# Kernel optimization log

Hardware: AMD Instinct MI355X
Metric: run time of the kernel (lower is better)

The kernel has to match this reference:

```python
import jax, jax.numpy as jnp
import numpy as np

NUM_LAYERS = 4  # -> 9 blocks: 4 encoder + bottleneck + 4 decoder
EPS = 1e-6
SQRT2 = float(np.sqrt(2.0))
INV_SQRT3 = float(1.0 / np.sqrt(3.0))


def _block(s, v, W0, W1, Wa, Wb):
    """_SelfInteractionUNet with full_square=False, irreps = Mx0e + Mx1o.

    tensor_square of per-channel (0e+1o):
      0e: s*s ; 0e: |v|^2/sqrt(3) ; 1o: sqrt(2)*s*v ; (2e is produced by e3nn
      but irreps_out has no 2e so the Linear discards it -> omitted here).
    """
    M = s.shape[-1]
    ts0a = s * s                                    # [N, M] 0e
    ts0b = jnp.sum(v * v, axis=-1) * INV_SQRT3      # [N, M] 0e
    ts1 = SQRT2 * s[..., None] * v                  # [N, M, 3] 1o
    s_in = jnp.concatenate([s, ts0a, ts0b], axis=-1)   # [N, 3M]
    v_in = jnp.concatenate([v, ts1], axis=1)           # [N, 2M, 3]
    # irreps-segmented Linear with path (fan-in) normalization
    s2 = (s_in @ W0) * (1.0 / np.sqrt(s_in.shape[-1]))               # [N, Mo]
    v2 = jnp.einsum('ncd,co->nod', v_in, W1) * (1.0 / np.sqrt(v_in.shape[1]))  # [N, Mo, 3]
    Mo = W0.shape[-1]
    # gated MLP on invariants (0e part), silu after each layer
    h = jax.nn.silu((s2 @ Wa) * (1.0 / np.sqrt(Mo)))                 # [N, Mo]
    g = jax.nn.silu((h @ Wb) * (1.0 / np.sqrt(Mo)))                  # [N, 2Mo]
    s2 = s2 * g[:, :Mo]
    v2 = v2 * g[:, Mo:, None]
    return s2, v2


def _eq_layernorm(s, v):
    # scalars: center + RMS normalize; vectors: norm-RMS normalize (equivariant)
    s = s - jnp.mean(s, axis=-1, keepdims=True)
    s = s * jax.lax.rsqrt(jnp.mean(s * s, axis=-1, keepdims=True) + EPS)
    v = v * jax.lax.rsqrt(jnp.mean(v * v, axis=(1, 2), keepdims=True) + EPS)
    return s, v


def _unet(scalars, vectors, W0, W1, Wa, Wb):
    s, v = scalars, vectors
    skips = []
    for i in range(NUM_LAYERS):
        s, v = _block(s, v, W0[i], W1[i], Wa[i], Wb[i])
        s, v = _eq_layernorm(s, v)
        skips.append((s, v))
    s, v = _block(s, v, W0[NUM_LAYERS], W1[NUM_LAYERS], Wa[NUM_LAYERS], Wb[NUM_LAYERS])
    for j in range(NUM_LAYERS):
        ss, vs = skips[NUM_LAYERS - 1 - j]
        s, v = s + ss, v + vs
        k = NUM_LAYERS + 1 + j
        s, v = _block(s, v, W0[k], W1[k], Wa[k], Wb[k])
        if j < NUM_LAYERS - 1:  # no norm on last decoder layer (norm_last=False)
            s, v = _eq_layernorm(s, v)
    N = s.shape[0]
    return jnp.concatenate([s, v.reshape(N, -1)], axis=-1)  # [N, 4M] irreps_array layout


def setup_inputs() -> dict:
    key = jax.random.key(0)
    ks = jax.random.split(key, 6)
    N, M = 16384, 256
    return {
        'scalars': jax.random.normal(ks[0], (N, M), jnp.float32),
        'vectors': jax.random.normal(ks[1], (N, M, 3), jnp.float32),
        'W0': jax.random.normal(ks[2], (9, 3 * M, M), jnp.float32),
        'W1': jax.random.normal(ks[3], (9, 2 * M, M), jnp.float32),
        'Wa': jax.random.normal(ks[4], (9, M, M), jnp.float32),
        'Wb': jax.random.normal(ks[5], (9, M, 2 * M), jnp.float32),
    }


def reference(scalars, vectors, W0, W1, Wa, Wb):
    return _unet(scalars, vectors, W0, W1, Wa, Wb)
```

## Files before the change

kernel.cpp:

```cpp
#include <hip/hip_runtime.h>
#include <hip/hip_bf16.h>
#include <math.h>


typedef __attribute__((ext_vector_type(8))) short bf16x8;
typedef __attribute__((ext_vector_type(4))) short bf16x4;
typedef __attribute__((ext_vector_type(4))) float f32x4;
typedef __attribute__((ext_vector_type(4))) _Float16 f16x4;

__device__ __forceinline__ unsigned asu(float f){ union{float f;unsigned u;}x; x.f=f; return x.u; }
__device__ __forceinline__ float asf(unsigned u){ union{unsigned u;float f;}x; x.u=u; return x.f; }

__device__ __forceinline__ unsigned short f2bf_r(float f){
  unsigned i = asu(f);
  return (unsigned short)((i + 0x7fffu + ((i >> 16) & 1u)) >> 16);
}
__device__ __forceinline__ float bf2f(unsigned short u){ return asf(((unsigned)u) << 16); }

__device__ __forceinline__ void split_t(float f, short& hi, short& lo){
  unsigned u = asu(f);
  hi = (short)(u >> 16);
  float lof = f - asf(u & 0xffff0000u);
  lo = (short)(asu(lof) >> 16);
}
__device__ __forceinline__ float rec(short h, short l){
  return asf(((unsigned)(unsigned short)h) << 16) + asf(((unsigned)(unsigned short)l) << 16);
}
__device__ __forceinline__ f32x4 rec4(const unsigned short* H, const unsigned short* L, size_t o){
  bf16x4 hv = *(const bf16x4*)(H + o);
  bf16x4 lv = *(const bf16x4*)(L + o);
  f32x4 f;
  #pragma unroll
  for (int j = 0; j < 4; ++j) f[j] = rec(hv[j], lv[j]);
  return f;
}

__device__ __forceinline__ int LO(int r, int kc){
  return r * 32 + ((((kc >> 3) ^ (r & 3)) << 3) | (kc & 7));
}

__global__ __launch_bounds__(256)
void transpose_w(const float* __restrict__ W, unsigned short* __restrict__ Wh,
                 unsigned short* __restrict__ Wl, int K, int Mo){
  __shared__ float tile[32][33];
  const int bi = blockIdx.z;
  const float* Wb = W + (size_t)bi * K * Mo;
  const size_t wo = (size_t)bi * K * Mo;
  const int k0 = blockIdx.x * 32, o0 = blockIdx.y * 32;
  const int tx = threadIdx.x & 31, ty = threadIdx.x >> 5;
  #pragma unroll
  for (int i = 0; i < 4; ++i){
    int k = ty + i * 8;
    tile[k][tx] = Wb[(size_t)(k0 + k) * Mo + o0 + tx];
  }
  __syncthreads();
  #pragma unroll
  for (int i = 0; i < 4; ++i){
    int o = ty + i * 8;
    float f = tile[tx][o];
    unsigned short h = f2bf_r(f);
    unsigned short l = f2bf_r(f - bf2f(h));
    Wh[wo + (size_t)(o0 + o) * K + k0 + tx] = h;
    Wl[wo + (size_t)(o0 + o) * K + k0 + tx] = l;
  }
}

__global__ __launch_bounds__(256)
void convert_inputs(const float* __restrict__ s, const float* __restrict__ v,
                    unsigned short* __restrict__ stH, unsigned short* __restrict__ stL,
                    int NM){
  int i = blockIdx.x * 256 + threadIdx.x;
  if (i >= NM) return;
  short h, l;
  split_t(s[i], h, l); stH[i] = h; stL[i] = l;
  const float* vp = v + (size_t)i * 3;
  #pragma unroll
  for (int d = 0; d < 3; ++d){
    split_t(vp[d], h, l);
    stH[(size_t)(1 + d) * NM + i] = h;
    stL[(size_t)(1 + d) * NM + i] = l;
  }
}

__global__ __launch_bounds__(512, 8)
void gemm_sv(const unsigned short* __restrict__ StH, const unsigned short* __restrict__ StL,
             const _Float16* __restrict__ skip,
             const unsigned short* __restrict__ W0h, const unsigned short* __restrict__ W0l,
             const unsigned short* __restrict__ W1h, const unsigned short* __restrict__ W1l,
             unsigned short* __restrict__ s2H, unsigned short* __restrict__ s2L,
             unsigned short* __restrict__ v2H, unsigned short* __restrict__ v2L,
             int NM, float cs, float cv)
{
  __shared__ unsigned short Ash[64*32], Asl[64*32], Bsh[256*32], Bsl[256*32];
  const int tid = threadIdx.x;
  const int lane = tid & 63, wave = tid >> 6;
  const int wm = (wave >> 2) * 32, wn = (wave & 3) * 64;
  const int row0 = blockIdx.x * 64;
  const int z = blockIdx.y;
  const bool isS = (z == 0);
  const int dv = z - 1;
  const int K = isS ? 768 : 512;
  const float scale = isS ? cs : cv;
  const unsigned short* Bhg = isS ? W0h : W1h;
  const unsigned short* Blg = isS ? W0l : W1l;
  unsigned short* outH = isS ? s2H : v2H + (size_t)dv * NM;
  unsigned short* outL = isS ? s2L : v2L + (size_t)dv * NM;
  const bool sk = (skip != nullptr);

  f32x4 acc[2][4];
  #pragma unroll
  for (int m = 0; m < 2; ++m){
    #pragma unroll
    for (int n = 0; n < 4; ++n) acc[m][n] = (f32x4){0.f,0.f,0.f,0.f};
  }

  const int bc = tid >> 1, bk = (tid & 1) * 16;
  const int ar = tid >> 3, ac = (tid & 7) * 4;

  for (int k0 = 0; k0 < K; k0 += 32){
    {
      const size_t o = (size_t)bc * K + k0 + bk;
      bf16x8 x0 = *(const bf16x8*)(Bhg + o);
      bf16x8 x1 = *(const bf16x8*)(Bhg + o + 8);
      bf16x8 y0 = *(const bf16x8*)(Blg + o);
      bf16x8 y1 = *(const bf16x8*)(Blg + o + 8);
      *(bf16x8*)(&Bsh[LO(bc, bk)])     = x0;
      *(bf16x8*)(&Bsh[LO(bc, bk + 8)]) = x1;
      *(bf16x8*)(&Bsl[LO(bc, bk)])     = y0;
      *(bf16x8*)(&Bsl[LO(bc, bk + 8)]) = y1;
    }
    {
      const int gr = row0 + ar;
      const int c  = (k0 + ac) & 255;
      const size_t o = (size_t)gr * 256 + c;
      const int seg = k0 >> 8;
      if (!sk && seg == 0){
        const int p = isS ? 0 : 1 + dv;
        *(bf16x4*)(&Ash[LO(ar, ac)]) = *(const bf16x4*)(StH + (size_t)p * NM + o);
        *(bf16x4*)(&Asl[LO(ar, ac)]) = *(const bf16x4*)(StL + (size_t)p * NM + o);
      } else {
        f32x4 f;
        if (isS){
          if (seg <= 1){
            f32x4 x = rec4(StH, StL, o);
            if (sk){
              f16x4 y = *(const f16x4*)(skip + o);
              #pragma unroll
              for (int j = 0; j < 4; ++j) x[j] += (float)y[j];
            }
            if (seg == 0){
              f = x;
            } else {
              #pragma unroll
              for (int j = 0; j < 4; ++j) f[j] = x[j] * x[j];
            }
          } else {
            f32x4 a0 = rec4(StH, StL, (size_t)NM + o);
            f32x4 a1 = rec4(StH, StL, (size_t)2*NM + o);
            f32x4 a2 = rec4(StH, StL, (size_t)3*NM + o);
            if (sk){
              f16x4 b0 = *(const f16x4*)(skip + (size_t)NM + o);
              f16x4 b1 = *(const f16x4*)(skip + (size_t)2*NM + o);
              f16x4 b2 = *(const f16x4*)(skip + (size_t)3*NM + o);
              #pragma unroll
              for (int j = 0; j < 4; ++j){
                a0[j] += (float)b0[j]; a1[j] += (float)b1[j]; a2[j] += (float)b2[j];
              }
            }
            #pragma unroll
            for (int j = 0; j < 4; ++j)
              f[j] = (a0[j]*a0[j] + a1[j]*a1[j] + a2[j]*a2[j]) * 0.57735026918962576f;
          }
        } else {
          f32x4 x = rec4(StH, StL, (size_t)(1 + dv)*NM + o);
          if (sk){
            f16x4 y = *(const f16x4*)(skip + (size_t)(1 + dv)*NM + o);
            #pragma unroll
            for (int j = 0; j < 4; ++j) x[j] += (float)y[j];
          }
          if (seg == 0){
            f = x;
          } else {
            f32x4 s = rec4(StH, StL, o);
            if (sk){
              f16x4 y = *(const f16x4*)(skip + o);
              #pragma unroll
              for (int j = 0; j < 4; ++j) s[j] += (float)y[j];
            }
            #pragma unroll
            for (int j = 0; j < 4; ++j) f[j] = 1.41421356237309505f * s[j] * x[j];
          }
        }
        bf16x4 hi, lo;
        #pragma unroll
        for (int j = 0; j < 4; ++j){ short h, l; split_t(f[j], h, l); hi[j]=h; lo[j]=l; }
        *(bf16x4*)(&Ash[LO(ar, ac)]) = hi;
        *(bf16x4*)(&Asl[LO(ar, ac)]) = lo;
      }
    }
    __syncthreads();

    const int arow = lane & 15;
    const int kq   = (lane >> 4) * 8;
    bf16x8 ah[2], al[2], bh[4], bl[4];
    #pragma unroll
    for (int m = 0; m < 2; ++m){
      const int r = wm + m*16 + arow;
      ah[m] = *(const bf16x8*)(&Ash[LO(r, kq)]);
      al[m] = *(const bf16x8*)(&Asl[LO(r, kq)]);
    }
    #pragma unroll
    for (int n = 0; n < 4; ++n){
      const int r = wn + n*16 + arow;
      bh[n] = *(const bf16x8*)(&Bsh[LO(r, kq)]);
      bl[n] = *(const bf16x8*)(&Bsl[LO(r, kq)]);
    }
    #pragma unroll
    for (int m = 0; m < 2; ++m){
      #pragma unroll
      for (int n = 0; n < 4; ++n){
        acc[m][n] = __builtin_amdgcn_mfma_f32_16x16x32_bf16(ah[m], bh[n], acc[m][n], 0, 0, 0);
        acc[m][n] = __builtin_amdgcn_mfma_f32_16x16x32_bf16(al[m], bh[n], acc[m][n], 0, 0, 0);
        acc[m][n] = __builtin_amdgcn_mfma_f32_16x16x32_bf16(ah[m], bl[n], acc[m][n], 0, 0, 0);
      }
    }
    __syncthreads();
  }

  #pragma unroll
  for (int m = 0; m < 2; ++m){
    #pragma unroll
    for (int n = 0; n < 4; ++n){
      const int cg = wn + n*16 + (lane & 15);
      #pragma unroll
      for (int j = 0; j < 4; ++j){
        const int rg = row0 + wm + m*16 + ((lane >> 4) * 4) + j;
        short h, l; split_t(acc[m][n][j] * scale, h, l);
        outH[(size_t)rg * 256 + cg] = (unsigned short)h;
        outL[(size_t)rg * 256 + cg] = (unsigned short)l;
      }
    }
  }
}

template<int EPI>
__global__ __launch_bounds__(512, 8)
void gemm_hg(const unsigned short* __restrict__ AhG, const unsigned short* __restrict__ AlG,
             const unsigned short* __restrict__ Bh, const unsigned short* __restrict__ Bl,
             int NM, float scale,
             unsigned short* __restrict__ outH, unsigned short* __restrict__ outL,
             const unsigned short* __restrict__ s2H, const unsigned short* __restrict__ s2L,
             const unsigned short* __restrict__ v2H, const unsigned short* __restrict__ v2L,
             unsigned short* __restrict__ stH, unsigned short* __restrict__ stL,
             float* __restrict__ fout)
{
  __shared__ unsigned short Ash[32*32], Asl[32*32], Bsh[256*32], Bsl[256*32];
  const int tid = threadIdx.x;
  const int lane = tid & 63, wave = tid >> 6;
  const int wm = (wave >> 2) * 16, wn = (wave & 3) * 64;
  const int row0 = blockIdx.x * 32;
  const int col0 = blockIdx.y * 256;
  const int K = 256;

  f32x4 acc[2][4];
  #pragma unroll
  for (int m = 0; m < 2; ++m){
    #pragma unroll
    for (int n = 0; n < 4; ++n) acc[m][n] = (f32x4){0.f,0.f,0.f,0.f};
  }

  const int bc = tid >> 1, bk = (tid & 1) * 16;

  for (int k0 = 0; k0 < K; k0 += 32){
    {
      const size_t o = (size_t)(col0 + bc) * K + k0 + bk;
      bf16x8 x0 = *(const bf16x8*)(Bh + o);
      bf16x8 x1 = *(const bf16x8*)(Bh + o + 8);
      bf16x8 y0 = *(const bf16x8*)(Bl + o);
      bf16x8 y1 = *(const bf16x8*)(Bl + o + 8);
      *(bf16x8*)(&Bsh[LO(bc, bk)])     = x0;
      *(bf16x8*)(&Bsh[LO(bc, bk + 8)]) = x1;
      *(bf16x8*)(&Bsl[LO(bc, bk)])     = y0;
      *(bf16x8*)(&Bsl[LO(bc, bk + 8)]) = y1;
    }
    if (tid < 256){
      const int ar = tid >> 3, ac = (tid & 7) * 4;
      const size_t o = (size_t)(row0 + ar) * 256 + k0 + ac;
      *(bf16x4*)(&Ash[LO(ar, ac)]) = *(const bf16x4*)(AhG + o);
      *(bf16x4*)(&Asl[LO(ar, ac)]) = *(const bf16x4*)(AlG + o);
    }
    __syncthreads();

    const int arow = lane & 15;
    const int kq   = (lane >> 4) * 8;
    bf16x8 ah, al, bh[4], bl[4];
    {
      const int r = wm + arow;
      ah = *(const bf16x8*)(&Ash[LO(r, kq)]);
      al = *(const bf16x8*)(&Asl[LO(r, kq)]);
    }
    #pragma unroll
    for (int n = 0; n < 4; ++n){
      const int r = wn + n*16 + arow;
      bh[n] = *(const bf16x8*)(&Bsh[LO(r, kq)]);
      bl[n] = *(const bf16x8*)(&Bsl[LO(r, kq)]);
    }
    #pragma unroll
    for (int n = 0; n < 4; ++n){
      acc[0][n] = __builtin_amdgcn_mfma_f32_16x16x32_bf16(ah, bh[n], acc[0][n], 0, 0, 0);
      acc[0][n] = __builtin_amdgcn_mfma_f32_16x16x32_bf16(al, bh[n], acc[0][n], 0, 0, 0);
      acc[0][n] = __builtin_amdgcn_mfma_f32_16x16x32_bf16(ah, bl[n], acc[0][n], 0, 0, 0);
    }
    __syncthreads();
  }

  #pragma unroll
  for (int n = 0; n < 4; ++n){
    const int cg = col0 + wn + n*16 + (lane & 15);
    #pragma unroll
    for (int j = 0; j < 4; ++j){
      const int rg = row0 + wm + ((lane >> 4) * 4) + j;
      float val = acc[0][n][j] * scale;
      if (EPI == 1){
        float sl = val / (1.f + expf(-val));
        short h, l; split_t(sl, h, l);
        outH[(size_t)rg * 256 + cg] = (unsigned short)h;
        outL[(size_t)rg * 256 + cg] = (unsigned short)l;
      } else {
        float gv = val / (1.f + expf(-val));
        if (cg < 256){
          const size_t o = (size_t)rg * 256 + cg;
          float sval = rec(s2H[o], s2L[o]) * gv;
          if (EPI == 2){
            short h, l; split_t(sval, h, l);
            stH[o] = (unsigned short)h; stL[o] = (unsigned short)l;
          } else {
            fout[(size_t)rg * 1024 + cg] = sval;
          }
        } else {
          const int c = cg - 256;
          #pragma unroll
          for (int d = 0; d < 3; ++d){
            const size_t o = (size_t)d * NM + (size_t)rg * 256 + c;
            float vv = rec(v2H[o], v2L[o]) * gv;
            if (EPI == 2){
              short h, l; split_t(vv, h, l);
              stH[(size_t)(1+d) * NM + (size_t)rg * 256 + c] = (unsigned short)h;
              stL[(size_t)(1+d) * NM + (size_t)rg * 256 + c] = (unsigned short)l;
            } else {
              fout[(size_t)rg * 1024 + 256 + 3 * (size_t)c + d] = vv;
            }
          }
        }
      }
    }
  }
}

__global__ __launch_bounds__(256)
void ln_k(unsigned short* __restrict__ stH, unsigned short* __restrict__ stL,
          _Float16* __restrict__ snap, int NM){
  const int row  = blockIdx.x * 4 + (threadIdx.x >> 6);
  const int lane = threadIdx.x & 63;
  const size_t o = (size_t)row * 256 + lane * 4;
  f32x4 sv = rec4(stH, stL, o);
  f32x4 v0 = rec4(stH, stL, (size_t)NM + o);
  f32x4 v1 = rec4(stH, stL, (size_t)2*NM + o);
  f32x4 v2 = rec4(stH, stL, (size_t)3*NM + o);
  float r0 = 0.f, r1 = 0.f, r2 = 0.f;
  #pragma unroll
  for (int j = 0; j < 4; ++j){
    r0 += sv[j];
    r1 += sv[j] * sv[j];
    r2 += v0[j]*v0[j] + v1[j]*v1[j] + v2[j]*v2[j];
  }
  #pragma unroll
  for (int off = 1; off < 64; off <<= 1){
    r0 += __shfl_xor(r0, off, 64);
    r1 += __shfl_xor(r1, off, 64);
    r2 += __shfl_xor(r2, off, 64);
  }
  float mu  = r0 * (1.f / 256.f);
  float var = r1 * (1.f / 256.f) - mu * mu;
  float srs = rsqrtf(var + 1e-6f);
  float vrs = rsqrtf(r2 * (1.f / 768.f) + 1e-6f);
  f32x4 pl[4];
  #pragma unroll
  for (int j = 0; j < 4; ++j){
    pl[0][j] = (sv[j] - mu) * srs;
    pl[1][j] = v0[j] * vrs; pl[2][j] = v1[j] * vrs; pl[3][j] = v2[j] * vrs;
  }
  #pragma unroll
  for (int p = 0; p < 4; ++p){
    bf16x4 hv, lv; f16x4 hx;
    #pragma unroll
    for (int j = 0; j < 4; ++j){
      short h, l; split_t(pl[p][j], h, l);
      hv[j] = h; lv[j] = l; hx[j] = (_Float16)pl[p][j];
    }
    *(bf16x4*)(stH + (size_t)p*NM + o) = hv;
    *(bf16x4*)(stL + (size_t)p*NM + o) = lv;
    if (snap) *(f16x4*)(snap + (size_t)p*NM + o) = hx;
  }
}

extern "C" void kernel_launch(void* const* d_in, const int* in_sizes, int n_in,
                              void* d_out, int out_size, void* d_ws, size_t ws_size,
                              hipStream_t stream){
  const float* s_in = (const float*)d_in[0];
  const float* v_in = (const float*)d_in[1];
  const float* W0 = (const float*)d_in[2];
  const float* W1 = (const float*)d_in[3];
  const float* Wa = (const float*)d_in[4];
  const float* Wb = (const float*)d_in[5];
  const int Mdim = 256;
  const int N  = in_sizes[0] / Mdim;
  const int NM = N * Mdim;

  unsigned short* ws = (unsigned short*)d_ws;
  size_t off = 0;
  auto alloc = [&](size_t elems){ unsigned short* p = ws + off; off += elems; return p; };
  unsigned short* W0h = alloc((size_t)9 * 768 * 256);
  unsigned short* W0l = alloc((size_t)9 * 768 * 256);
  unsigned short* W1h = alloc((size_t)9 * 512 * 256);
  unsigned short* W1l = alloc((size_t)9 * 512 * 256);
  unsigned short* Wah = alloc((size_t)9 * 256 * 256);
  unsigned short* Wal = alloc((size_t)9 * 256 * 256);
  unsigned short* Wbh = alloc((size_t)9 * 256 * 512);
  unsigned short* Wbl = alloc((size_t)9 * 256 * 512);
  unsigned short* s2H = alloc(NM);
  unsigned short* s2L = alloc(NM);
  unsigned short* v2H = alloc((size_t)3 * NM);
  unsigned short* v2L = alloc((size_t)3 * NM);
  unsigned short* hH  = alloc(NM);
  unsigned short* hL  = alloc(NM);
  _Float16* skips = (_Float16*)(ws + off);
  (void)ws_size;

  unsigned short* stateH = (unsigned short*)d_out;
  unsigned short* stateL = stateH + (size_t)4 * NM;

  dim3 blk(256);
  dim3 blk5(512);
  transpose_w<<<dim3(768/32, 256/32, 9), blk, 0, stream>>>(W0, W0h, W0l, 768, 256);
  transpose_w<<<dim3(512/32, 256/32, 9), blk, 0, stream>>>(W1, W1h, W1l, 512, 256);
  transpose_w<<<dim3(256/32, 256/32, 9), blk, 0, stream>>>(Wa, Wah, Wal, 256, 256);
  transpose_w<<<dim3(256/32, 512/32, 9), blk, 0, stream>>>(Wb, Wbh, Wbl, 256, 512);
  convert_inputs<<<dim3(NM/256), blk, 0, stream>>>(s_in, v_in, stateH, stateL, NM);

  const float c_s2 = 1.f / sqrtf(768.f);
  const float c_v2 = 1.f / sqrtf(512.f);
  const float c_hg = 1.f / 16.f;

  auto run_block = [&](int i, const _Float16* skip, bool fin){
    const unsigned short* w0h = W0h + (size_t)i * 768 * 256;
    const unsigned short* w0l = W0l + (size_t)i * 768 * 256;
    const unsigned short* w1h = W1h + (size_t)i * 512 * 256;
    const unsigned short* w1l = W1l + (size_t)i * 512 * 256;
    const unsigned short* wah = Wah + (size_t)i * 256 * 256;
    const unsigned short* wal = Wal + (size_t)i * 256 * 256;
    const unsigned short* wbh = Wbh + (size_t)i * 256 * 512;
    const unsigned short* wbl = Wbl + (size_t)i * 256 * 512;
    gemm_sv<<<dim3(N/64, 4), blk5, 0, stream>>>(stateH, stateL, skip,
                                                w0h, w0l, w1h, w1l,
                                                s2H, s2L, v2H, v2L, NM, c_s2, c_v2);
    gemm_hg<1><<<dim3(N/32, 1), blk5, 0, stream>>>(s2H, s2L, wah, wal, NM, c_hg,
                                                   hH, hL, nullptr, nullptr, nullptr, nullptr,
                                                   nullptr, nullptr, nullptr);
    if (!fin)
      gemm_hg<2><<<dim3(N/32, 2), blk5, 0, stream>>>(hH, hL, wbh, wbl, NM, c_hg,
                                                     nullptr, nullptr, s2H, s2L, v2H, v2L,
                                                     stateH, stateL, nullptr);
    else
      gemm_hg<3><<<dim3(N/32, 2), blk5, 0, stream>>>(hH, hL, wbh, wbl, NM, c_hg,
                                                     nullptr, nullptr, s2H, s2L, v2H, v2L,
                                                     nullptr, nullptr, (float*)d_out);
  };

  for (int i = 0; i < 4; ++i){
    run_block(i, nullptr, false);
    ln_k<<<dim3(N/4), blk, 0, stream>>>(stateH, stateL, skips + (size_t)i * 4 * NM, NM);
  }
  run_block(4, nullptr, false);
  for (int j = 0; j < 4; ++j){
    run_block(5 + j, skips + (size_t)(3 - j) * 4 * NM, j == 3);
    if (j < 3) ln_k<<<dim3(N/4), blk, 0, stream>>>(stateH, stateL, nullptr, NM);
  }
}
```

Measured before the change: 2.413 ms.

## Double GEMM row tiles, pad LDS rows, and use nontemporal global accesses

Doubles the M tile of gemm_sv (64 to 128 rows) and gemm_hg (32 to 64 rows) so each B tile loaded into LDS is reused across more rows. This halves the grid and lowers launch-bound occupancy to 4. The XOR-swizzled LDS layout is replaced by rows padded to stride 40, and the MFMA loop now loads A fragments per m. Most global loads and stores of activations and state become nontemporal, to keep the streaming traffic out of cache. The cost is more registers for the accumulators, more LDS, and fewer resident waves.

After: 3.778 ms. 1.57x slower.

```diff
diff --git a/kernel.cpp b/kernel.cpp
--- a/kernel.cpp
+++ b/kernel.cpp
@@ -26,18 +26,26 @@
 __device__ __forceinline__ float rec(short h, short l){
   return asf(((unsigned)(unsigned short)h) << 16) + asf(((unsigned)(unsigned short)l) << 16);
 }
-__device__ __forceinline__ f32x4 rec4(const unsigned short* H, const unsigned short* L, size_t o){
-  bf16x4 hv = *(const bf16x4*)(H + o);
-  bf16x4 lv = *(const bf16x4*)(L + o);
+
+__device__ __forceinline__ bf16x8 ntl8(const unsigned short* p){
+  return __builtin_nontemporal_load((const bf16x8*)p);
+}
+__device__ __forceinline__ bf16x4 ntl4(const unsigned short* p){
+  return __builtin_nontemporal_load((const bf16x4*)p);
+}
+__device__ __forceinline__ f16x4 ntlh(const _Float16* p){
+  return __builtin_nontemporal_load((const f16x4*)p);
+}
+__device__ __forceinline__ f32x4 rec4nt(const unsigned short* H, const unsigned short* L, size_t o){
+  bf16x4 hv = ntl4(H + o);
+  bf16x4 lv = ntl4(L + o);
   f32x4 f;
   #pragma unroll
   for (int j = 0; j < 4; ++j) f[j] = rec(hv[j], lv[j]);
   return f;
 }
 
-__device__ __forceinline__ int LO(int r, int kc){
-  return r * 32 + ((((kc >> 3) ^ (r & 3)) << 3) | (kc & 7));
-}
+__device__ __forceinline__ int LO(int r, int kc){ return r * 40 + kc; }
 
 __global__ __launch_bounds__(256)
 void transpose_w(const float* __restrict__ W, unsigned short* __restrict__ Wh,
@@ -82,7 +90,7 @@
   }
 }
 
-__global__ __launch_bounds__(512, 8)
+__global__ __launch_bounds__(512, 4)
 void gemm_sv(const unsigned short* __restrict__ StH, const unsigned short* __restrict__ StL,
              const _Float16* __restrict__ skip,
              const unsigned short* __restrict__ W0h, const unsigned short* __restrict__ W0l,
@@ -91,11 +99,11 @@
              unsigned short* __restrict__ v2H, unsigned short* __restrict__ v2L,
              int NM, float cs, float cv)
 {
-  __shared__ unsigned short Ash[64*32], Asl[64*32], Bsh[256*32], Bsl[256*32];
+  __shared__ unsigned short Ash[128*40], Asl[128*40], Bsh[256*40], Bsl[256*40];
   const int tid = threadIdx.x;
   const int lane = tid & 63, wave = tid >> 6;
-  const int wm = (wave >> 2) * 32, wn = (wave & 3) * 64;
-  const int row0 = blockIdx.x * 64;
+  const int wm = (wave >> 2) * 64, wn = (wave & 3) * 64;
+  const int row0 = blockIdx.x * 128;
   const int z = blockIdx.y;
   const bool isS = (z == 0);
   const int dv = z - 1;
@@ -107,17 +115,18 @@
   unsigned short* outL = isS ? s2L : v2L + (size_t)dv * NM;
   const bool sk = (skip != nullptr);
 
-  f32x4 acc[2][4];
-  #pragma unroll
-  for (int m = 0; m < 2; ++m){
+  f32x4 acc[4][4];
+  #pragma unroll
+  for (int m = 0; m < 4; ++m){
     #pragma unroll
     for (int n = 0; n < 4; ++n) acc[m][n] = (f32x4){0.f,0.f,0.f,0.f};
   }
 
   const int bc = tid >> 1, bk = (tid & 1) * 16;
-  const int ar = tid >> 3, ac = (tid & 7) * 4;
+  const int ar = tid >> 2, ac = (tid & 3) * 8;
 
   for (int k0 = 0; k0 < K; k0 += 32){
+    const int seg = k0 >> 8;
     {
       const size_t o = (size_t)bc * K + k0 + bk;
       bf16x8 x0 = *(const bf16x8*)(Bhg + o);
@@ -133,82 +142,79 @@
       const int gr = row0 + ar;
       const int c  = (k0 + ac) & 255;
       const size_t o = (size_t)gr * 256 + c;
-      const int seg = k0 >> 8;
       if (!sk && seg == 0){
         const int p = isS ? 0 : 1 + dv;
-        *(bf16x4*)(&Ash[LO(ar, ac)]) = *(const bf16x4*)(StH + (size_t)p * NM + o);
-        *(bf16x4*)(&Asl[LO(ar, ac)]) = *(const bf16x4*)(StL + (size_t)p * NM + o);
+        *(bf16x8*)(&Ash[LO(ar, ac)]) = ntl8(StH + (size_t)p * NM + o);
+        *(bf16x8*)(&Asl[LO(ar, ac)]) = ntl8(StL + (size_t)p * NM + o);
       } else {
-        f32x4 f;
-        if (isS){
-          if (seg <= 1){
-            f32x4 x = rec4(StH, StL, o);
+        #pragma unroll
+        for (int q = 0; q < 2; ++q){
+          const size_t oq = o + 4 * q;
+          f32x4 f;
+          if (isS){
+            if (seg <= 1){
+              f32x4 x = rec4nt(StH, StL, oq);
+              if (sk){
+                f16x4 y = ntlh(skip + oq);
+                #pragma unroll
+                for (int j = 0; j < 4; ++j) x[j] += (float)y[j];
+              }
+              if (seg == 0){
+                f = x;
+              } else {
+                #pragma unroll
+                for (int j = 0; j < 4; ++j) f[j] = x[j] * x[j];
+              }
+            } else {
+              f32x4 a0 = rec4nt(StH, StL, (size_t)NM + oq);
+              f32x4 a1 = rec4nt(StH, StL, (size_t)2*NM + oq);
+              f32x4 a2 = rec4nt(StH, StL, (size_t)3*NM + oq);
+              if (sk){
+                f16x4 b0 = ntlh(skip + (size_t)NM + oq);
+                f16x4 b1 = ntlh(skip + (size_t)2*NM + oq);
+                f16x4 b2 = ntlh(skip + (size_t)3*NM + oq);
+                #pragma unroll
+                for (int j = 0; j < 4; ++j){
+                  a0[j] += (float)b0[j]; a1[j] += (float)b1[j]; a2[j] += (float)b2[j];
+                }
+              }
+              #pragma unroll
+              for (int j = 0; j < 4; ++j)
+                f[j] = (a0[j]*a0[j] + a1[j]*a1[j] + a2[j]*a2[j]) * 0.57735026918962576f;
+            }
+          } else {
+            f32x4 x = rec4nt(StH, StL, (size_t)(1 + dv)*NM + oq);
             if (sk){
-              f16x4 y = *(const f16x4*)(skip + o);
+              f16x4 y = ntlh(skip + (size_t)(1 + dv)*NM + oq);
               #pragma unroll
               for (int j = 0; j < 4; ++j) x[j] += (float)y[j];
             }
             if (seg == 0){
               f = x;
             } else {
+              f32x4 s = rec4nt(StH, StL, oq);
+              if (sk){
+                f16x4 y = ntlh(skip + oq);
+                #pragma unroll
+                for (int j = 0; j < 4; ++j) s[j] += (float)y[j];
+              }
               #pragma unroll
-              for (int j = 0; j < 4; ++j) f[j] = x[j] * x[j];
+              for (int j = 0; j < 4; ++j) f[j] = 1.41421356237309505f * s[j] * x[j];
             }
-          } else {
-            f32x4 a0 = rec4(StH, StL, (size_t)NM + o);
-            f32x4 a1 = rec4(StH, StL, (size_t)2*NM + o);
-            f32x4 a2 = rec4(StH, StL, (size_t)3*NM + o);
-            if (sk){
-              f16x4 b0 = *(const f16x4*)(skip + (size_t)NM + o);
-              f16x4 b1 = *(const f16x4*)(skip + (size_t)2*NM + o);
-              f16x4 b2 = *(const f16x4*)(skip + (size_t)3*NM + o);
-              #pragma unroll
-              for (int j = 0; j < 4; ++j){
-                a0[j] += (float)b0[j]; a1[j] += (float)b1[j]; a2[j] += (float)b2[j];
-              }
-            }
-            #pragma unroll
-            for (int j = 0; j < 4; ++j)
-              f[j] = (a0[j]*a0[j] + a1[j]*a1[j] + a2[j]*a2[j]) * 0.57735026918962576f;
           }
-        } else {
-          f32x4 x = rec4(StH, StL, (size_t)(1 + dv)*NM + o);
-          if (sk){
-            f16x4 y = *(const f16x4*)(skip + (size_t)(1 + dv)*NM + o);
-            #pragma unroll
-            for (int j = 0; j < 4; ++j) x[j] += (float)y[j];
-          }
-          if (seg == 0){
-            f = x;
-          } else {
-            f32x4 s = rec4(StH, StL, o);
-            if (sk){
-              f16x4 y = *(const f16x4*)(skip + o);
-              #pragma unroll
-              for (int j = 0; j < 4; ++j) s[j] += (float)y[j];
-            }
-            #pragma unroll
-            for (int j = 0; j < 4; ++j) f[j] = 1.41421356237309505f * s[j] * x[j];
-          }
+          bf16x4 hi, lo;
+          #pragma unroll
+          for (int j = 0; j < 4; ++j){ short h, l; split_t(f[j], h, l); hi[j]=h; lo[j]=l; }
+          *(bf16x4*)(&Ash[LO(ar, ac + 4*q)]) = hi;
+          *(bf16x4*)(&Asl[LO(ar, ac + 4*q)]) = lo;
         }
-        bf16x4 hi, lo;
-        #pragma unroll
-        for (int j = 0; j < 4; ++j){ short h, l; split_t(f[j], h, l); hi[j]=h; lo[j]=l; }
-        *(bf16x4*)(&Ash[LO(ar, ac)]) = hi;
-        *(bf16x4*)(&Asl[LO(ar, ac)]) = lo;
       }
     }
     __syncthreads();
 
     const int arow = lane & 15;
     const int kq   = (lane >> 4) * 8;
-    bf16x8 ah[2], al[2], bh[4], bl[4];
-    #pragma unroll
-    for (int m = 0; m < 2; ++m){
-      const int r = wm + m*16 + arow;
-      ah[m] = *(const bf16x8*)(&Ash[LO(r, kq)]);
-      al[m] = *(const bf16x8*)(&Asl[LO(r, kq)]);
-    }
+    bf16x8 bh[4], bl[4];
     #pragma unroll
     for (int n = 0; n < 4; ++n){
       const int r = wn + n*16 + arow;
@@ -216,19 +222,25 @@
       bl[n] = *(const bf16x8*)(&Bsl[LO(r, kq)]);
     }
     #pragma unroll
-    for (int m = 0; m < 2; ++m){
-      #pragma unroll
-      for (int n = 0; n < 4; ++n){
-        acc[m][n] = __builtin_amdgcn_mfma_f32_16x16x32_bf16(ah[m], bh[n], acc[m][n], 0, 0, 0);
-        acc[m][n] = __builtin_amdgcn_mfma_f32_16x16x32_bf16(al[m], bh[n], acc[m][n], 0, 0, 0);
-        acc[m][n] = __builtin_amdgcn_mfma_f32_16x16x32_bf16(ah[m], bl[n], acc[m][n], 0, 0, 0);
-      }
+    for (int m = 0; m < 4; ++m){
+      const int r = wm + m*16 + arow;
+      bf16x8 ah = *(const bf16x8*)(&Ash[LO(r, kq)]);
+      bf16x8 al = *(const bf16x8*)(&Asl[LO(r, kq)]);
+      #pragma unroll
+      for (int n = 0; n < 4; ++n)
+        acc[m][n] = __builtin_amdgcn_mfma_f32_16x16x32_bf16(ah, bh[n], acc[m][n], 0, 0, 0);
+      #pragma unroll
+      for (int n = 0; n < 4; ++n)
+        acc[m][n] = __builtin_amdgcn_mfma_f32_16x16x32_bf16(al, bh[n], acc[m][n], 0, 0, 0);
+      #pragma unroll
+      for (int n = 0; n < 4; ++n)
+        acc[m][n] = __builtin_amdgcn_mfma_f32_16x16x32_bf16(ah, bl[n], acc[m][n], 0, 0, 0);
     }
     __syncthreads();
   }
 
   #pragma unroll
-  for (int m = 0; m < 2; ++m){
+  for (int m = 0; m < 4; ++m){
     #pragma unroll
     for (int n = 0; n < 4; ++n){
       const int cg = wn + n*16 + (lane & 15);
@@ -236,15 +248,15 @@
       for (int j = 0; j < 4; ++j){
         const int rg = row0 + wm + m*16 + ((lane >> 4) * 4) + j;
         short h, l; split_t(acc[m][n][j] * scale, h, l);
-        outH[(size_t)rg * 256 + cg] = (unsigned short)h;
-        outL[(size_t)rg * 256 + cg] = (unsigned short)l;
+        __builtin_nontemporal_store((unsigned short)h, &outH[(size_t)rg * 256 + cg]);
+        __builtin_nontemporal_store((unsigned short)l, &outL[(size_t)rg * 256 + cg]);
       }
     }
   }
 }
 
 template<int EPI>
-__global__ __launch_bounds__(512, 8)
+__global__ __launch_bounds__(512, 4)
 void gemm_hg(const unsigned short* __restrict__ AhG, const unsigned short* __restrict__ AlG,
              const unsigned short* __restrict__ Bh, const unsigned short* __restrict__ Bl,
              int NM, float scale,
@@ -254,11 +266,11 @@
              unsigned short* __restrict__ stH, unsigned short* __restrict__ stL,
              float* __restrict__ fout)
 {
-  __shared__ unsigned short Ash[32*32], Asl[32*32], Bsh[256*32], Bsl[256*32];
+  __shared__ unsigned short Ash[64*40], Asl[64*40], Bsh[256*40], Bsl[256*40];
   const int tid = threadIdx.x;
   const int lane = tid & 63, wave = tid >> 6;
-  const int wm = (wave >> 2) * 16, wn = (wave & 3) * 64;
-  const int row0 = blockIdx.x * 32;
+  const int wm = (wave >> 2) * 32, wn = (wave & 3) * 64;
+  const int row0 = blockIdx.x * 64;
   const int col0 = blockIdx.y * 256;
   const int K = 256;
 
@@ -270,6 +282,7 @@
   }
 
   const int bc = tid >> 1, bk = (tid & 1) * 16;
+  const int ar = tid >> 3, acx = (tid & 7) * 4;
 
   for (int k0 = 0; k0 < K; k0 += 32){
     {
@@ -283,22 +296,16 @@
       *(bf16x8*)(&Bsl[LO(bc, bk)])     = y0;
       *(bf16x8*)(&Bsl[LO(bc, bk + 8)]) = y1;
     }
-    if (tid < 256){
-      const int ar = tid >> 3, ac = (tid & 7) * 4;
-      const size_t o = (size_t)(row0 + ar) * 256 + k0 + ac;
-      *(bf16x4*)(&Ash[LO(ar, ac)]) = *(const bf16x4*)(AhG + o);
-      *(bf16x4*)(&Asl[LO(ar, ac)]) = *(const bf16x4*)(AlG + o);
+    {
+      const size_t o = (size_t)(row0 + ar) * 256 + k0 + acx;
+      *(bf16x4*)(&Ash[LO(ar, acx)]) = ntl4(AhG + o);
+      *(bf16x4*)(&Asl[LO(ar, acx)]) = ntl4(AlG + o);
     }
     __syncthreads();
 
     const int arow = lane & 15;
     const int kq   = (lane >> 4) * 8;
-    bf16x8 ah, al, bh[4], bl[4];
-    {
-      const int r = wm + arow;
-      ah = *(const bf16x8*)(&Ash[LO(r, kq)]);
-      al = *(const bf16x8*)(&Asl[LO(r, kq)]);
-    }
+    bf16x8 bh[4], bl[4];
     #pragma unroll
     for (int n = 0; n < 4; ++n){
       const int r = wn + n*16 + arow;
@@ -306,49 +313,64 @@
       bl[n] = *(const bf16x8*)(&Bsl[LO(r, kq)]);
     }
     #pragma unroll
+    for (int m = 0; m < 2; ++m){
+      const int r = wm + m*16 + arow;
+      bf16x8 ah = *(const bf16x8*)(&Ash[LO(r, kq)]);
+      bf16x8 al = *(const bf16x8*)(&Asl[LO(r, kq)]);
+      #pragma unroll
+      for (int n = 0; n < 4; ++n)
+        acc[m][n] = __builtin_amdgcn_mfma_f32_16x16x32_bf16(ah, bh[n], acc[m][n], 0, 0, 0);
+      #pragma unroll
+      for (int n = 0; n < 4; ++n)
+        acc[m][n] = __builtin_amdgcn_mfma_f32_16x16x32_bf16(al, bh[n], acc[m][n], 0, 0, 0);
+      #pragma unroll
+      for (int n = 0; n < 4; ++n)
+        acc[m][n] = __builtin_amdgcn_mfma_f32_16x16x32_bf16(ah, bl[n], acc[m][n], 0, 0, 0);
+    }
+    __syncthreads();
+  }
+
+  #pragma unroll
+  for (int m = 0; m < 2; ++m){
+    #pragma unroll
     for (int n = 0; n < 4; ++n){
-      acc[0][n] = __builtin_amdgcn_mfma_f32_16x16x32_bf16(ah, bh[n], acc[0][n], 0, 0, 0);
-      acc[0][n] = __builtin_amdgcn_mfma_f32_16x16x32_bf16(al, bh[n], acc[0][n], 0, 0, 0);
-      acc[0][n] = __builtin_amdgcn_mfma_f32_16x16x32_bf16(ah, bl[n], acc[0][n], 0, 0, 0);
-    }
-    __syncthreads();
-  }
-
-  #pragma unroll
-  for (int n = 0; n < 4; ++n){
-    const int cg = col0 + wn + n*16 + (lane & 15);
-    #pragma unroll
-    for (int j = 0; j < 4; ++j){
-      const int rg = row0 + wm + ((lane >> 4) * 4) + j;
-      float val = acc[0][n][j] * scale;
-      if (EPI == 1){
-        float sl = val / (1.f + expf(-val));
-        short h, l; split_t(sl, h, l);
-        outH[(size_t)rg * 256 + cg] = (unsigned short)h;
-        outL[(size_t)rg * 256 + cg] = (unsigned short)l;
-      } else {
-        float gv = val / (1.f + expf(-val));
-        if (cg < 256){
-          const size_t o = (size_t)rg * 256 + cg;
-          float sval = rec(s2H[o], s2L[o]) * gv;
-          if (EPI == 2){
-            short h, l; split_t(sval, h, l);
-            stH[o] = (unsigned short)h; stL[o] = (unsigned short)l;
+      const int cg = col0 + wn + n*16 + (lane & 15);
+      #pragma unroll
+      for (int j = 0; j < 4; ++j){
+        const int rg = row0 + wm + m*16 + ((lane >> 4) * 4) + j;
+        float val = acc[m][n][j] * scale;
+        if (EPI == 1){
+          float sl = val / (1.f + expf(-val));
+          short h, l; split_t(sl, h, l);
+          __builtin_nontemporal_store((unsigned short)h, &outH[(size_t)rg * 256 + cg]);
+          __builtin_nontemporal_store((unsigned short)l, &outL[(size_t)rg * 256 + cg]);
+        } else {
+          float gv = val / (1.f + expf(-val));
+          if (cg < 256){
+            const size_t o = (size_t)rg * 256 + cg;
+            float sval = rec((short)__builtin_nontemporal_load(&s2H[o]),
+                             (short)__builtin_nontemporal_load(&s2L[o])) * gv;
+            if (EPI == 2){
+              short h, l; split_t(sval, h, l);
+              __builtin_nontemporal_store((unsigned short)h, &stH[o]);
+              __builtin_nontemporal_store((unsigned short)l, &stL[o]);
+            } else {
+              __builtin_nontemporal_store(sval, &fout[(size_t)rg * 1024 + cg]);
+            }
           } else {
-            fout[(size_t)rg * 1024 + cg] = sval;
-          }
-        } else {
-          const int c = cg - 256;
-          #pragma unroll
-          for (int d = 0; d < 3; ++d){
-            const size_t o = (size_t)d * NM + (size_t)rg * 256 + c;
-            float vv = rec(v2H[o], v2L[o]) * gv;
-            if (EPI == 2){
-              short h, l; split_t(vv, h, l);
-              stH[(size_t)(1+d) * NM + (size_t)rg * 256 + c] = (unsigned short)h;
-              stL[(size_t)(1+d) * NM + (size_t)rg * 256 + c] = (unsigned short)l;
-            } else {
-              fout[(size_t)rg * 1024 + 256 + 3 * (size_t)c + d] = vv;
+            const int c = cg - 256;
+            #pragma unroll
+            for (int d = 0; d < 3; ++d){
+              const size_t o = (size_t)d * NM + (size_t)rg * 256 + c;
+              float vv = rec((short)__builtin_nontemporal_load(&v2H[o]),
+                             (short)__builtin_nontemporal_load(&v2L[o])) * gv;
+              if (EPI == 2){
+                short h, l; split_t(vv, h, l);
+                __builtin_nontemporal_store((unsigned short)h, &stH[(size_t)(1+d) * NM + (size_t)rg * 256 + c]);
+                __builtin_nontemporal_store((unsigned short)l, &stL[(size_t)(1+d) * NM + (size_t)rg * 256 + c]);
+              } else {
+                __builtin_nontemporal_store(vv, &fout[(size_t)rg * 1024 + 256 + 3 * (size_t)c + d]);
+              }
             }
           }
         }
@@ -363,10 +385,10 @@
   const int row  = blockIdx.x * 4 + (threadIdx.x >> 6);
   const int lane = threadIdx.x & 63;
   const size_t o = (size_t)row * 256 + lane * 4;
-  f32x4 sv = rec4(stH, stL, o);
-  f32x4 v0 = rec4(stH, stL, (size_t)NM + o);
-  f32x4 v1 = rec4(stH, stL, (size_t)2*NM + o);
-  f32x4 v2 = rec4(stH, stL, (size_t)3*NM + o);
+  f32x4 sv = rec4nt(stH, stL, o);
+  f32x4 v0 = rec4nt(stH, stL, (size_t)NM + o);
+  f32x4 v1 = rec4nt(stH, stL, (size_t)2*NM + o);
+  f32x4 v2 = rec4nt(stH, stL, (size_t)3*NM + o);
   float r0 = 0.f, r1 = 0.f, r2 = 0.f;
   #pragma unroll
   for (int j = 0; j < 4; ++j){
@@ -398,9 +420,9 @@
       short h, l; split_t(pl[p][j], h, l);
       hv[j] = h; lv[j] = l; hx[j] = (_Float16)pl[p][j];
     }
-    *(bf16x4*)(stH + (size_t)p*NM + o) = hv;
-    *(bf16x4*)(stL + (size_t)p*NM + o) = lv;
-    if (snap) *(f16x4*)(snap + (size_t)p*NM + o) = hx;
+    __builtin_nontemporal_store(hv, (bf16x4*)(stH + (size_t)p*NM + o));
+    __builtin_nontemporal_store(lv, (bf16x4*)(stL + (size_t)p*NM + o));
+    if (snap) __builtin_nontemporal_store(hx, (f16x4*)(snap + (size_t)p*NM + o));
   }
 }
 
@@ -461,18 +483,18 @@
     const unsigned short* wal = Wal + (size_t)i * 256 * 256;
     const unsigned short* wbh = Wbh + (size_t)i * 256 * 512;
     const unsigned short* wbl = Wbl + (size_t)i * 256 * 512;
-    gemm_sv<<<dim3(N/64, 4), blk5, 0, stream>>>(stateH, stateL, skip,
-                                                w0h, w0l, w1h, w1l,
-                                                s2H, s2L, v2H, v2L, NM, c_s2, c_v2);
-    gemm_hg<1><<<dim3(N/32, 1), blk5, 0, stream>>>(s2H, s2L, wah, wal, NM, c_hg,
+    gemm_sv<<<dim3(N/128, 4), blk5, 0, stream>>>(stateH, stateL, skip,
+                                                 w0h, w0l, w1h, w1l,
+                                                 s2H, s2L, v2H, v2L, NM, c_s2, c_v2);
+    gemm_hg<1><<<dim3(N/64, 1), blk5, 0, stream>>>(s2H, s2L, wah, wal, NM, c_hg,
                                                    hH, hL, nullptr, nullptr, nullptr, nullptr,
                                                    nullptr, nullptr, nullptr);
     if (!fin)
-      gemm_hg<2><<<dim3(N/32, 2), blk5, 0, stream>>>(hH, hL, wbh, wbl, NM, c_hg,
+      gemm_hg<2><<<dim3(N/64, 2), blk5, 0, stream>>>(hH, hL, wbh, wbl, NM, c_hg,
                                                      nullptr, nullptr, s2H, s2L, v2H, v2L,
                                                      stateH, stateL, nullptr);
     else
-      gemm_hg<3><<<dim3(N/32, 2), blk5, 0, stream>>>(hH, hL, wbh, wbl, NM, c_hg,
+      gemm_hg<3><<<dim3(N/64, 2), blk5, 0, stream>>>(hH, hL, wbh, wbl, NM, c_hg,
                                                      nullptr, nullptr, s2H, s2L, v2H, v2L,
                                                      nullptr, nullptr, (float*)d_out);
   };
```

## Retile GEMMs to 128x128 blocks with padded LDS layout

Applied to the files above, without the earlier changes.

Both GEMM kernels switch from wide-N, short-M tiles (64x256 and 32x256 with 512 threads) to square 128x128 tiles with 256 threads, where each wave computes a 64x64 sub-tile using 4x4 MFMA fragments. The XOR-swizzled LDS index is replaced by a row stride padded to 40 elements. Square tiles are meant to improve operand reuse per LDS load and cut redundant global reads of A across column blocks. The cost is more accumulator registers per thread, lower occupancy, and a larger LDS footprint.

After: 2.419 ms. Within noise of the previous version (+0.3%).

```diff
diff --git a/kernel.cpp b/kernel.cpp
--- a/kernel.cpp
+++ b/kernel.cpp
@@ -35,9 +35,7 @@
   return f;
 }
 
-__device__ __forceinline__ int LO(int r, int kc){
-  return r * 32 + ((((kc >> 3) ^ (r & 3)) << 3) | (kc & 7));
-}
+__device__ __forceinline__ int LO(int r, int kc){ return r * 40 + kc; }
 
 __global__ __launch_bounds__(256)
 void transpose_w(const float* __restrict__ W, unsigned short* __restrict__ Wh,
@@ -82,7 +80,7 @@
   }
 }
 
-__global__ __launch_bounds__(512, 8)
+__global__ __launch_bounds__(256, 4)
 void gemm_sv(const unsigned short* __restrict__ StH, const unsigned short* __restrict__ StL,
              const _Float16* __restrict__ skip,
              const unsigned short* __restrict__ W0h, const unsigned short* __restrict__ W0l,
@@ -91,14 +89,15 @@
              unsigned short* __restrict__ v2H, unsigned short* __restrict__ v2L,
              int NM, float cs, float cv)
 {
-  __shared__ unsigned short Ash[64*32], Asl[64*32], Bsh[256*32], Bsl[256*32];
+  __shared__ unsigned short Ash[128*40], Asl[128*40], Bsh[128*40], Bsl[128*40];
   const int tid = threadIdx.x;
   const int lane = tid & 63, wave = tid >> 6;
-  const int wm = (wave >> 2) * 32, wn = (wave & 3) * 64;
-  const int row0 = blockIdx.x * 64;
+  const int wm = (wave >> 1) * 64, wn = (wave & 1) * 64;
+  const int row0 = blockIdx.x * 128;
   const int z = blockIdx.y;
-  const bool isS = (z == 0);
-  const int dv = z - 1;
+  const bool isS = (z < 2);
+  const int dv = (z - 2) >> 1;
+  const int col0 = isS ? z * 128 : ((z - 2) & 1) * 128;
   const int K = isS ? 768 : 512;
   const float scale = isS ? cs : cv;
   const unsigned short* Bhg = isS ? W0h : W1h;
@@ -107,38 +106,43 @@
   unsigned short* outL = isS ? s2L : v2L + (size_t)dv * NM;
   const bool sk = (skip != nullptr);
 
-  f32x4 acc[2][4];
-  #pragma unroll
-  for (int m = 0; m < 2; ++m){
+  f32x4 acc[4][4];
+  #pragma unroll
+  for (int m = 0; m < 4; ++m){
     #pragma unroll
     for (int n = 0; n < 4; ++n) acc[m][n] = (f32x4){0.f,0.f,0.f,0.f};
   }
 
-  const int bc = tid >> 1, bk = (tid & 1) * 16;
-  const int ar = tid >> 3, ac = (tid & 7) * 4;
-
   for (int k0 = 0; k0 < K; k0 += 32){
-    {
-      const size_t o = (size_t)bc * K + k0 + bk;
-      bf16x8 x0 = *(const bf16x8*)(Bhg + o);
-      bf16x8 x1 = *(const bf16x8*)(Bhg + o + 8);
-      bf16x8 y0 = *(const bf16x8*)(Blg + o);
-      bf16x8 y1 = *(const bf16x8*)(Blg + o + 8);
-      *(bf16x8*)(&Bsh[LO(bc, bk)])     = x0;
-      *(bf16x8*)(&Bsh[LO(bc, bk + 8)]) = x1;
-      *(bf16x8*)(&Bsl[LO(bc, bk)])     = y0;
-      *(bf16x8*)(&Bsl[LO(bc, bk + 8)]) = y1;
-    }
-    {
-      const int gr = row0 + ar;
-      const int c  = (k0 + ac) & 255;
-      const size_t o = (size_t)gr * 256 + c;
-      const int seg = k0 >> 8;
-      if (!sk && seg == 0){
-        const int p = isS ? 0 : 1 + dv;
-        *(bf16x4*)(&Ash[LO(ar, ac)]) = *(const bf16x4*)(StH + (size_t)p * NM + o);
-        *(bf16x4*)(&Asl[LO(ar, ac)]) = *(const bf16x4*)(StL + (size_t)p * NM + o);
-      } else {
+    const int seg = k0 >> 8;
+    #pragma unroll
+    for (int it = 0; it < 2; ++it){
+      int idx = tid + it * 256;
+      int r = idx >> 2, kc = (idx & 3) * 8;
+      const size_t o = (size_t)(col0 + r) * K + k0 + kc;
+      *(bf16x8*)(&Bsh[LO(r, kc)]) = *(const bf16x8*)(Bhg + o);
+      *(bf16x8*)(&Bsl[LO(r, kc)]) = *(const bf16x8*)(Blg + o);
+    }
+    if (!sk && seg == 0){
+      const int p = isS ? 0 : 1 + dv;
+      const unsigned short* SH = StH + (size_t)p * NM;
+      const unsigned short* SL = StL + (size_t)p * NM;
+      #pragma unroll
+      for (int it = 0; it < 2; ++it){
+        int idx = tid + it * 256;
+        int r = idx >> 2, kc = (idx & 3) * 8;
+        const size_t o = (size_t)(row0 + r) * 256 + k0 + kc;
+        *(bf16x8*)(&Ash[LO(r, kc)]) = *(const bf16x8*)(SH + o);
+        *(bf16x8*)(&Asl[LO(r, kc)]) = *(const bf16x8*)(SL + o);
+      }
+    } else {
+      #pragma unroll
+      for (int it = 0; it < 4; ++it){
+        int idx = tid + it * 256;
+        int r = idx >> 3, c4 = (idx & 7) * 4;
+        const int gr = row0 + r;
+        const int c = (k0 + c4) & 255;
+        const size_t o = (size_t)gr * 256 + c;
         f32x4 f;
         if (isS){
           if (seg <= 1){
@@ -194,17 +198,17 @@
         bf16x4 hi, lo;
         #pragma unroll
         for (int j = 0; j < 4; ++j){ short h, l; split_t(f[j], h, l); hi[j]=h; lo[j]=l; }
-        *(bf16x4*)(&Ash[LO(ar, ac)]) = hi;
-        *(bf16x4*)(&Asl[LO(ar, ac)]) = lo;
+        *(bf16x4*)(&Ash[LO(r, c4)]) = hi;
+        *(bf16x4*)(&Asl[LO(r, c4)]) = lo;
       }
     }
     __syncthreads();
 
     const int arow = lane & 15;
     const int kq   = (lane >> 4) * 8;
-    bf16x8 ah[2], al[2], bh[4], bl[4];
-    #pragma unroll
-    for (int m = 0; m < 2; ++m){
+    bf16x8 ah[4], al[4], bh[4], bl[4];
+    #pragma unroll
+    for (int m = 0; m < 4; ++m){
       const int r = wm + m*16 + arow;
       ah[m] = *(const bf16x8*)(&Ash[LO(r, kq)]);
       al[m] = *(const bf16x8*)(&Asl[LO(r, kq)]);
@@ -216,7 +220,7 @@
       bl[n] = *(const bf16x8*)(&Bsl[LO(r, kq)]);
     }
     #pragma unroll
-    for (int m = 0; m < 2; ++m){
+    for (int m = 0; m < 4; ++m){
       #pragma unroll
       for (int n = 0; n < 4; ++n){
         acc[m][n] = __builtin_amdgcn_mfma_f32_16x16x32_bf16(ah[m], bh[n], acc[m][n], 0, 0, 0);
@@ -228,10 +232,10 @@
   }
 
   #pragma unroll
-  for (int m = 0; m < 2; ++m){
+  for (int m = 0; m < 4; ++m){
     #pragma unroll
     for (int n = 0; n < 4; ++n){
-      const int cg = wn + n*16 + (lane & 15);
+      const int cg = col0 + wn + n*16 + (lane & 15);
       #pragma unroll
       for (int j = 0; j < 4; ++j){
         const int rg = row0 + wm + m*16 + ((lane >> 4) * 4) + j;
@@ -244,7 +248,7 @@
 }
 
 template<int EPI>
-__global__ __launch_bounds__(512, 8)
+__global__ __launch_bounds__(256, 4)
 void gemm_hg(const unsigned short* __restrict__ AhG, const unsigned short* __restrict__ AlG,
              const unsigned short* __restrict__ Bh, const unsigned short* __restrict__ Bl,
              int NM, float scale,
@@ -254,50 +258,47 @@
              unsigned short* __restrict__ stH, unsigned short* __restrict__ stL,
              float* __restrict__ fout)
 {
-  __shared__ unsigned short Ash[32*32], Asl[32*32], Bsh[256*32], Bsl[256*32];
+  __shared__ unsigned short Ash[128*40], Asl[128*40], Bsh[128*40], Bsl[128*40];
   const int tid = threadIdx.x;
   const int lane = tid & 63, wave = tid >> 6;
-  const int wm = (wave >> 2) * 16, wn = (wave & 3) * 64;
-  const int row0 = blockIdx.x * 32;
-  const int col0 = blockIdx.y * 256;
+  const int wm = (wave >> 1) * 64, wn = (wave & 1) * 64;
+  const int row0 = blockIdx.x * 128;
+  const int col0 = blockIdx.y * 128;
   const int K = 256;
 
-  f32x4 acc[2][4];
-  #pragma unroll
-  for (int m = 0; m < 2; ++m){
+  f32x4 acc[4][4];
+  #pragma unroll
+  for (int m = 0; m < 4; ++m){
     #pragma unroll
     for (int n = 0; n < 4; ++n) acc[m][n] = (f32x4){0.f,0.f,0.f,0.f};
   }
 
-  const int bc = tid >> 1, bk = (tid & 1) * 16;
-
   for (int k0 = 0; k0 < K; k0 += 32){
-    {
-      const size_t o = (size_t)(col0 + bc) * K + k0 + bk;
-      bf16x8 x0 = *(const bf16x8*)(Bh + o);
-      bf16x8 x1 = *(const bf16x8*)(Bh + o + 8);
-      bf16x8 y0 = *(const bf16x8*)(Bl + o);
-      bf16x8 y1 = *(const bf16x8*)(Bl + o + 8);
-      *(bf16x8*)(&Bsh[LO(bc, bk)])     = x0;
-      *(bf16x8*)(&Bsh[LO(bc, bk + 8)]) = x1;
-      *(bf16x8*)(&Bsl[LO(bc, bk)])     = y0;
-      *(bf16x8*)(&Bsl[LO(bc, bk + 8)]) = y1;
-    }
-    if (tid < 256){
-      const int ar = tid >> 3, ac = (tid & 7) * 4;
-      const size_t o = (size_t)(row0 + ar) * 256 + k0 + ac;
-      *(bf16x4*)(&Ash[LO(ar, ac)]) = *(const bf16x4*)(AhG + o);
-      *(bf16x4*)(&Asl[LO(ar, ac)]) = *(const bf16x4*)(AlG + o);
+    #pragma unroll
+    for (int it = 0; it < 2; ++it){
+      int idx = tid + it * 256;
+      int r = idx >> 2, kc = (idx & 3) * 8;
+      {
+        const size_t o = (size_t)(col0 + r) * K + k0 + kc;
+        *(bf16x8*)(&Bsh[LO(r, kc)]) = *(const bf16x8*)(Bh + o);
+        *(bf16x8*)(&Bsl[LO(r, kc)]) = *(const bf16x8*)(Bl + o);
+      }
+      {
+        const size_t o = (size_t)(row0 + r) * 256 + k0 + kc;
+        *(bf16x8*)(&Ash[LO(r, kc)]) = *(const bf16x8*)(AhG + o);
+        *(bf16x8*)(&Asl[LO(r, kc)]) = *(const bf16x8*)(AlG + o);
+      }
     }
     __syncthreads();
 
     const int arow = lane & 15;
     const int kq   = (lane >> 4) * 8;
-    bf16x8 ah, al, bh[4], bl[4];
-    {
-      const int r = wm + arow;
-      ah = *(const bf16x8*)(&Ash[LO(r, kq)]);
-      al = *(const bf16x8*)(&Asl[LO(r, kq)]);
+    bf16x8 ah[4], al[4], bh[4], bl[4];
+    #pragma unroll
+    for (int m = 0; m < 4; ++m){
+      const int r = wm + m*16 + arow;
+      ah[m] = *(const bf16x8*)(&Ash[LO(r, kq)]);
+      al[m] = *(const bf16x8*)(&Asl[LO(r, kq)]);
     }
     #pragma unroll
     for (int n = 0; n < 4; ++n){
@@ -306,49 +307,55 @@
       bl[n] = *(const bf16x8*)(&Bsl[LO(r, kq)]);
     }
     #pragma unroll
+    for (int m = 0; m < 4; ++m){
+      #pragma unroll
+      for (int n = 0; n < 4; ++n){
+        acc[m][n] = __builtin_amdgcn_mfma_f32_16x16x32_bf16(ah[m], bh[n], acc[m][n], 0, 0, 0);
+        acc[m][n] = __builtin_amdgcn_mfma_f32_16x16x32_bf16(al[m], bh[n], acc[m][n], 0, 0, 0);
+        acc[m][n] = __builtin_amdgcn_mfma_f32_16x16x32_bf16(ah[m], bl[n], acc[m][n], 0, 0, 0);
+      }
+    }
+    __syncthreads();
+  }
+
+  #pragma unroll
+  for (int m = 0; m < 4; ++m){
+    #pragma unroll
     for (int n = 0; n < 4; ++n){
-      acc[0][n] = __builtin_amdgcn_mfma_f32_16x16x32_bf16(ah, bh[n], acc[0][n], 0, 0, 0);
-      acc[0][n] = __builtin_amdgcn_mfma_f32_16x16x32_bf16(al, bh[n], acc[0][n], 0, 0, 0);
-      acc[0][n] = __builtin_amdgcn_mfma_f32_16x16x32_bf16(ah, bl[n], acc[0][n], 0, 0, 0);
-    }
-    __syncthreads();
-  }
-
-  #pragma unroll
-  for (int n = 0; n < 4; ++n){
-    const int cg = col0 + wn + n*16 + (lane & 15);
-    #pragma unroll
-    for (int j = 0; j < 4; ++j){
-      const int rg = row0 + wm + ((lane >> 4) * 4) + j;
-      float val = acc[0][n][j] * scale;
-      if (EPI == 1){
-        float sl = val / (1.f + expf(-val));
-        short h, l; split_t(sl, h, l);
-        outH[(size_t)rg * 256 + cg] = (unsigned short)h;
-        outL[(size_t)rg * 256 + cg] = (unsigned short)l;
-      } else {
-        float gv = val / (1.f + expf(-val));
-        if (cg < 256){
-          const size_t o = (size_t)rg * 256 + cg;
-          float sval = rec(s2H[o], s2L[o]) * gv;
-          if (EPI == 2){
-            short h, l; split_t(sval, h, l);
-            stH[o] = (unsigned short)h; stL[o] = (unsigned short)l;
+      const int cg = col0 + wn + n*16 + (lane & 15);
+      #pragma unroll
+      for (int j = 0; j < 4; ++j){
+        const int rg = row0 + wm + m*16 + ((lane >> 4) * 4) + j;
+        float val = acc[m][n][j] * scale;
+        if (EPI == 1){
+          float sl = val / (1.f + expf(-val));
+          short h, l; split_t(sl, h, l);
+          outH[(size_t)rg * 256 + cg] = (unsigned short)h;
+          outL[(size_t)rg * 256 + cg] = (unsigned short)l;
+        } else {
+          float gv = val / (1.f + expf(-val));
+          if (cg < 256){
+            const size_t o = (size_t)rg * 256 + cg;
+            float sval = rec((short)s2H[o], (short)s2L[o]) * gv;
+            if (EPI == 2){
+              short h, l; split_t(sval, h, l);
+              stH[o] = (unsigned short)h; stL[o] = (unsigned short)l;
+            } else {
+              fout[(size_t)rg * 1024 + cg] = sval;
+            }
           } else {
-            fout[(size_t)rg * 1024 + cg] = sval;
-          }
-        } else {
-          const int c = cg - 256;
-          #pragma unroll
-          for (int d = 0; d < 3; ++d){
-            const size_t o = (size_t)d * NM + (size_t)rg * 256 + c;
-            float vv = rec(v2H[o], v2L[o]) * gv;
-            if (EPI == 2){
-              short h, l; split_t(vv, h, l);
-              stH[(size_t)(1+d) * NM + (size_t)rg * 256 + c] = (unsigned short)h;
-              stL[(size_t)(1+d) * NM + (size_t)rg * 256 + c] = (unsigned short)l;
-            } else {
-              fout[(size_t)rg * 1024 + 256 + 3 * (size_t)c + d] = vv;
+            const int c = cg - 256;
+            #pragma unroll
+            for (int d = 0; d < 3; ++d){
+              const size_t o = (size_t)d * NM + (size_t)rg * 256 + c;
+              float vv = rec((short)v2H[o], (short)v2L[o]) * gv;
+              if (EPI == 2){
+                short h, l; split_t(vv, h, l);
+                stH[(size_t)(1+d) * NM + (size_t)rg * 256 + c] = (unsigned short)h;
+                stL[(size_t)(1+d) * NM + (size_t)rg * 256 + c] = (unsigned short)l;
+              } else {
+                fout[(size_t)rg * 1024 + 256 + 3 * (size_t)c + d] = vv;
+              }
             }
           }
         }
@@ -441,7 +448,6 @@
   unsigned short* stateL = stateH + (size_t)4 * NM;
 
   dim3 blk(256);
-  dim3 blk5(512);
   transpose_w<<<dim3(768/32, 256/32, 9), blk, 0, stream>>>(W0, W0h, W0l, 768, 256);
   transpose_w<<<dim3(512/32, 256/32, 9), blk, 0, stream>>>(W1, W1h, W1l, 512, 256);
   transpose_w<<<dim3(256/32, 256/32, 9), blk, 0, stream>>>(Wa, Wah, Wal, 256, 256);
@@ -451,6 +457,7 @@
   const float c_s2 = 1.f / sqrtf(768.f);
   const float c_v2 = 1.f / sqrtf(512.f);
   const float c_hg = 1.f / 16.f;
+  const int gx = N / 128;
 
   auto run_block = [&](int i, const _Float16* skip, bool fin){
     const unsigned short* w0h = W0h + (size_t)i * 768 * 256;
@@ -461,20 +468,20 @@
     const unsigned short* wal = Wal + (size_t)i * 256 * 256;
     const unsigned short* wbh = Wbh + (size_t)i * 256 * 512;
     const unsigned short* wbl = Wbl + (size_t)i * 256 * 512;
-    gemm_sv<<<dim3(N/64, 4), blk5, 0, stream>>>(stateH, stateL, skip,
-                                                w0h, w0l, w1h, w1l,
-                                                s2H, s2L, v2H, v2L, NM, c_s2, c_v2);
-    gemm_hg<1><<<dim3(N/32, 1), blk5, 0, stream>>>(s2H, s2L, wah, wal, NM, c_hg,
-                                                   hH, hL, nullptr, nullptr, nullptr, nullptr,
-                                                   nullptr, nullptr, nullptr);
+    gemm_sv<<<dim3(gx, 8), blk, 0, stream>>>(stateH, stateL, skip,
+                                             w0h, w0l, w1h, w1l,
+                                             s2H, s2L, v2H, v2L, NM, c_s2, c_v2);
+    gemm_hg<1><<<dim3(gx, 2), blk, 0, stream>>>(s2H, s2L, wah, wal, NM, c_hg,
+                                                hH, hL, nullptr, nullptr, nullptr, nullptr,
+                                                nullptr, nullptr, nullptr);
     if (!fin)
-      gemm_hg<2><<<dim3(N/32, 2), blk5, 0, stream>>>(hH, hL, wbh, wbl, NM, c_hg,
-                                                     nullptr, nullptr, s2H, s2L, v2H, v2L,
-                                                     stateH, stateL, nullptr);
+      gemm_hg<2><<<dim3(gx, 4), blk, 0, stream>>>(hH, hL, wbh, wbl, NM, c_hg,
+                                                  nullptr, nullptr, s2H, s2L, v2H, v2L,
+                                                  stateH, stateL, nullptr);
     else
-      gemm_hg<3><<<dim3(N/32, 2), blk5, 0, stream>>>(hH, hL, wbh, wbl, NM, c_hg,
-                                                     nullptr, nullptr, s2H, s2L, v2H, v2L,
-                                                     nullptr, nullptr, (float*)d_out);
+      gemm_hg<3><<<dim3(gx, 4), blk, 0, stream>>>(hH, hL, wbh, wbl, NM, c_hg,
+                                                  nullptr, nullptr, s2H, s2L, v2H, v2L,
+                                                  nullptr, nullptr, (float*)d_out);
   };
 
   for (int i = 0; i < 4; ++i){
```
